# Performance work log

Hardware: AMD Instinct MI355X
Metric: run time of the kernel (lower is better)

The kernel has to match this reference:

```python
import jax, jax.numpy as jnp
import numpy as np

HEADS = 6
WS = 16          # window_size
OWS = 24         # overlap_win_size
DIM = 192
TABLE = (WS + OWS - 1) ** 2  # 1521


def setup_inputs() -> dict:
    key = jax.random.key(0)
    k1, k2, k3, k4, k5, k6 = jax.random.split(key, 6)
    b = 256
    nq = WS * WS          # 256
    n = OWS * OWS         # 576
    x_q = jax.random.normal(k1, (b, nq, DIM), dtype=jnp.float32)
    x_kv = jax.random.normal(k2, (b, n, DIM), dtype=jnp.float32)
    rpi = jax.random.randint(k3, (nq, n), 0, TABLE, dtype=jnp.int64)
    Wq = jax.random.normal(k4, (DIM, DIM), dtype=jnp.float32) * 0.02
    Wkv = jax.random.normal(k5, (2 * DIM, DIM), dtype=jnp.float32) * 0.02
    bias_table = jax.random.normal(k6, (TABLE, HEADS), dtype=jnp.float32) * 0.02
    return {"x_q": x_q, "x_kv": x_kv, "rpi": rpi, "Wq": Wq, "Wkv": Wkv, "bias_table": bias_table}


def reference(x_q, x_kv, rpi, Wq, Wkv, bias_table):
    b, nq, dim = x_q.shape
    n = x_kv.shape[1]
    hd = dim // HEADS
    scale = hd ** (-0.5)

    # projections (torch Linear: y = x @ W^T)
    q = (x_q @ Wq.T).reshape(b, nq, HEADS, hd).transpose(0, 2, 1, 3)      # b h nq d
    kv = x_kv @ Wkv.T                                                    # b n 2*dim
    k, v = jnp.split(kv, 2, axis=-1)
    k = k.reshape(b, n, HEADS, hd).transpose(0, 2, 1, 3)                  # b h n d
    v = v.reshape(b, n, HEADS, hd).transpose(0, 2, 1, 3)                  # b h n d

    attn = scale * jnp.einsum('bhqd,bhkd->bhqk', q, k)                    # b h nq n

    # gathered relative-position bias: table[rpi] -> (nq, n, h)
    rpb = bias_table[rpi.reshape(-1)].reshape(nq, n, HEADS)
    # nq < n branch in source: permute(2, 0, 1) -> (h, nq, n)
    rpb = rpb.transpose(2, 0, 1)

    attn = jax.nn.softmax(attn + rpb[None], axis=-1)
    out = jnp.einsum('bhqk,bhkd->bhqd', attn, v)                          # b h nq d
    out = out.transpose(0, 2, 1, 3).reshape(b, nq, dim)
    return out
```

## Files before the change

### kernel.cpp

```cpp
#include <hip/hip_runtime.h>
#include <cstdint>

typedef unsigned short u16;
typedef short s16x8 __attribute__((ext_vector_type(8)));
typedef float f32x4 __attribute__((ext_vector_type(4)));
typedef float f32x16 __attribute__((ext_vector_type(16)));

#if __has_builtin(__builtin_amdgcn_exp2f)
#define EXP2(x) __builtin_amdgcn_exp2f(x)
#else
#define EXP2(x) __expf((x)*0.6931471805599453f)
#endif

__device__ __forceinline__ u16 f2bf(float x) {
  uint32_t u = __builtin_bit_cast(uint32_t, x);
  u += 0x7FFFu + ((u >> 16) & 1u);
  return (u16)(u >> 16);
}
__device__ __forceinline__ float bf2f(u16 v) {
  return __builtin_bit_cast(float, (uint32_t)v << 16);
}
__device__ __forceinline__ uint32_t pk_bf16(float lo, float hi) {
  uint32_t ul = __builtin_bit_cast(uint32_t, lo);
  uint32_t uh = __builtin_bit_cast(uint32_t, hi);
  ul += 0x7FFFu + ((ul >> 16) & 1u);
  uh += 0x7FFFu + ((uh >> 16) & 1u);
  return __builtin_amdgcn_perm(uh, ul, 0x07060302u);
}
__device__ __forceinline__ f32x4 mfma16(s16x8 a, s16x8 b, f32x4 c) {
  return __builtin_amdgcn_mfma_f32_16x16x32_bf16(a, b, c, 0, 0, 0);
}
__device__ __forceinline__ f32x16 mfma32(s16x8 a, s16x8 b, f32x16 c) {
  return __builtin_amdgcn_mfma_f32_32x32x16_bf16(a, b, c, 0, 0, 0);
}
__device__ __forceinline__ s16x8 ld_frag(const u16* p) {
  uint4 v = *(const uint4*)p;
  return __builtin_bit_cast(s16x8, v);
}

__global__ void prep_w(const float* __restrict__ Wq, const float* __restrict__ Wkv,
                       u16* __restrict__ wqs, u16* __restrict__ wkvs) {
  int tid = blockIdx.x * 256 + threadIdx.x;
  if (tid >= 13824) return;
  bool isQ = tid < 4608;
  int id = isQ ? tid : tid - 4608;
  int lane = id & 63, fk = id >> 6;
  int kk = fk % 6, fb = fk / 6;
  int f = fb * 16 + (lane & 15), k0 = kk * 32 + ((lane >> 4) << 3);
  const float* src = (isQ ? Wq : Wkv) + (size_t)f * 192 + k0;
  const float sc = isQ ? 0.2550348583f : 1.0f;
  float4 a = ((const float4*)src)[0], b = ((const float4*)src)[1];
  uint4 o;
  o.x = pk_bf16(a.x * sc, a.y * sc); o.y = pk_bf16(a.z * sc, a.w * sc);
  o.z = pk_bf16(b.x * sc, b.y * sc); o.w = pk_bf16(b.z * sc, b.w * sc);
  *(uint4*)&(isQ ? wqs : wkvs)[(size_t)id * 8] = o;
}

__global__ void build_rpb(const int* __restrict__ rpi, const float* __restrict__ table,
                          u16* __restrict__ rpb) {
  const int bi = blockIdx.x;
  const int h = bi / 18, kt = bi - h * 18;
  const int t = threadIdx.x, lane = t & 63, w = t >> 6;
  const int u = lane >> 5, l31 = lane & 31;
  const int q = (w << 5) + l31;
  const int n0 = (kt << 5) + (u << 2);
  u16 vals[16];
#pragma unroll
  for (int g = 0; g < 4; ++g) {
    int4 id4 = *(const int4*)&rpi[q * 576 + n0 + (g << 3)];
    vals[(g << 2) + 0] = f2bf(table[id4.x * 6 + h] * 1.4426950409f);
    vals[(g << 2) + 1] = f2bf(table[id4.y * 6 + h] * 1.4426950409f);
    vals[(g << 2) + 2] = f2bf(table[id4.z * 6 + h] * 1.4426950409f);
    vals[(g << 2) + 3] = f2bf(table[id4.w * 6 + h] * 1.4426950409f);
  }
  uint4* dst = (uint4*)&rpb[((size_t)bi * 512 + t) * 16];
  dst[0] = *(uint4*)&vals[0];
  dst[1] = *(uint4*)&vals[8];
}

template <int NC, int MODE>
__device__ __forceinline__ void proj_body(const float* __restrict__ A,
                                          const u16* __restrict__ W,
                                          u16* __restrict__ outQ, u16* __restrict__ outK,
                                          u16* __restrict__ outV, int blk,
                                          u16* __restrict__ lAf) {
  const int t = threadIdx.x, lane = t & 63, w = t >> 6, c = lane & 15, hi = lane >> 4;
  const int mbase0 = blk << 7;
#pragma unroll
  for (int p = 0; p < 2; ++p) {
    const int row = (p << 6) + (t >> 2), cq = t & 3;
    const int fr = row >> 4, cc = row & 15;
    const float* src = A + (size_t)(mbase0 + row) * 192 + (cq << 2);
    const int e0 = (cq & 1) << 2;
#pragma unroll
    for (int i = 0; i < 12; ++i) {
      float4 v = *(const float4*)(src + (i << 4));
      const int kk = i >> 1, h2 = ((i & 1) << 1) + (cq >> 1);
      uint2 pv;
      pv.x = pk_bf16(v.x, v.y);
      pv.y = pk_bf16(v.z, v.w);
      *(uint2*)&lAf[((((fr * 6 + kk) << 6) + (h2 << 4) + cc) << 3) + e0] = pv;
    }
  }
  __syncthreads();
  s16x8 af[2][6];
#pragma unroll
  for (int rg = 0; rg < 2; ++rg)
#pragma unroll
    for (int kk = 0; kk < 6; ++kk)
      af[rg][kk] = ld_frag(&lAf[((((((w << 1) + rg) * 6 + kk) << 6) + lane) << 3)]);

  constexpr int TOT = NC * 6;
  s16x8 wB[3][4];
#pragma unroll
  for (int s0 = 0; s0 < 2; ++s0) {
#pragma unroll
    for (int nb = 0; nb < 4; ++nb)
      wB[s0][nb] = ld_frag(&W[((size_t)((nb * 6 + s0) * 64 + lane)) * 8]);
  }
  f32x4 acc[2][4];
#pragma unroll
  for (int rg = 0; rg < 2; ++rg)
#pragma unroll
    for (int nb = 0; nb < 4; ++nb) acc[rg][nb] = f32x4{0.f, 0.f, 0.f, 0.f};
#pragma unroll
  for (int s = 0; s < TOT; ++s) {
    const int nc = s / 6, kk = s % 6;
    if (s + 2 < TOT) {
      const int s2 = s + 2, nc2 = s2 / 6, kk2 = s2 % 6;
#pragma unroll
      for (int nb = 0; nb < 4; ++nb)
        wB[s2 % 3][nb] = ld_frag(&W[((size_t)((((nc2 << 2) + nb) * 6 + kk2) * 64 + lane)) * 8]);
    }
#pragma unroll
    for (int rg = 0; rg < 2; ++rg)
#pragma unroll
      for (int nb = 0; nb < 4; ++nb)
        acc[rg][nb] = mfma16(wB[s % 3][nb], af[rg][kk], acc[rg][nb]);
    if (kk == 5) {
#pragma unroll
      for (int rg = 0; rg < 2; ++rg) {
        const int m = mbase0 + (w << 5) + (rg << 4) + c;
#pragma unroll
        for (int nb = 0; nb < 4; ++nb) {
          int fb = (nc << 6) + (nb << 4) + (hi << 2);
          uint2 pv;
          pv.x = pk_bf16(acc[rg][nb][0], acc[rg][nb][1]);
          pv.y = pk_bf16(acc[rg][nb][2], acc[rg][nb][3]);
          if (MODE == 0) {
            int b = m >> 8, q = m & 255, hh = fb >> 5, d = fb & 31;
            *(uint2*)&outQ[((((size_t)(b * 6 + hh)) << 8) + q) * 32 + d] = pv;
          } else {
            int b = m / 576, tok = m - b * 576;
            if (fb >= 192) {
              int f2 = fb - 192, hh = f2 >> 5, d = f2 & 31;
              *(uint2*)&outV[(((size_t)(b * 6 + hh)) * 576 + tok) * 32 + d] = pv;
            } else {
              int hh = fb >> 5, dd = fb & 31;
              int half = dd >> 4, uu = (dd >> 3) & 1, e0 = dd & 7;
              int ktt = tok >> 5, lt = tok & 31;
              *(uint2*)&outK[(size_t)((b * 6 + hh) * 18 + ktt) * 1024 +
                             half * 512 + uu * 256 + lt * 8 + e0] = pv;
            }
          }
          acc[rg][nb] = f32x4{0.f, 0.f, 0.f, 0.f};
        }
      }
    }
  }
}

__launch_bounds__(256)
__global__ void proj_all(const float* __restrict__ xq, const float* __restrict__ xkv,
                         const u16* __restrict__ wqs, const u16* __restrict__ wkvs,
                         u16* __restrict__ Qws, u16* __restrict__ Kws,
                         u16* __restrict__ Vws) {
  __shared__ __align__(16) u16 lAf[24576];
  int blk = blockIdx.x;
  if (blk < 512) proj_body<3, 0>(xq, wqs, Qws, nullptr, nullptr, blk, lAf);
  else           proj_body<6, 1>(xkv, wkvs, nullptr, Kws, Vws, blk - 512, lAf);
}

#define VSTR 600
__launch_bounds__(512)
__global__ void attn(const u16* __restrict__ Qws, const u16* __restrict__ Kws,
                     const u16* __restrict__ Vws, const u16* __restrict__ rpb,
                     float* __restrict__ out) {
  __shared__ __align__(16) u16 Vt[32 * VSTR];
  const int bh = blockIdx.x, b = bh / 6, h = bh - b * 6;
  const size_t kvbase = (size_t)bh * 576 * 32;
  const int t = threadIdx.x;
  for (int key = t; key < 576; key += 512) {
    int kk = key & 31, k15 = kk & 15;
    int p = ((kk >> 4) << 4) | (((k15 >> 2) & 1) << 3) | ((k15 >> 3) << 2) | (k15 & 3);
    int col = ((key >> 5) << 5) + p;
    const uint4* src = (const uint4*)&Vws[kvbase + (size_t)key * 32];
    uint4 r[4] = {src[0], src[1], src[2], src[3]};
    const u16* vs = (const u16*)r;
#pragma unroll
    for (int d = 0; d < 32; ++d) Vt[d * VSTR + col] = vs[d];
  }
  const int lane = t & 63, l31 = lane & 31, u = lane >> 5, w = t >> 6;
  const int qg = (w << 5) + l31;
  s16x8 qf[2];
#pragma unroll
  for (int m = 0; m < 2; ++m)
    qf[m] = ld_frag(&Qws[((size_t)bh * 256 + qg) * 32 + (m << 4) + (u << 3)]);
  __syncthreads();
  f32x16 oacc;
#pragma unroll
  for (int r = 0; r < 16; ++r) oacc[r] = 0.f;
  float psum = 0.f;
  const u16* kfb = Kws + (size_t)bh * 18432 + (size_t)lane * 8;
  const u16* bp0 = rpb + (size_t)h * 147456 + (size_t)t * 16;
  s16x8 kA[2], kB[2];
  uint4 bA[2], bB[2];
  kA[0] = ld_frag(kfb);        kB[0] = ld_frag(kfb + 512);
  kA[1] = ld_frag(kfb + 1024); kB[1] = ld_frag(kfb + 1536);
  bA[0] = *(const uint4*)(bp0);        bB[0] = *(const uint4*)(bp0 + 8);
  bA[1] = *(const uint4*)(bp0 + 8192); bB[1] = *(const uint4*)(bp0 + 8192 + 8);
#pragma unroll 2
  for (int kt = 0; kt < 18; ++kt) {
    const int k0 = kt << 5, cur = kt & 1;
    s16x8 vf0 = ld_frag(&Vt[l31 * VSTR + k0 + (u << 3)]);
    s16x8 vf1 = ld_frag(&Vt[l31 * VSTR + k0 + 16 + (u << 3)]);
    f32x16 st;
#pragma unroll
    for (int r = 0; r < 16; ++r) st[r] = 0.f;
    st = mfma32(kA[cur], qf[0], st);
    st = mfma32(kB[cur], qf[1], st);
    uint4 bAc = bA[cur], bBc = bB[cur];
    if (kt < 16) {
      kA[cur] = ld_frag(kfb + (size_t)(kt + 2) * 1024);
      kB[cur] = ld_frag(kfb + (size_t)(kt + 2) * 1024 + 512);
      bA[cur] = *(const uint4*)(bp0 + (size_t)(kt + 2) * 8192);
      bB[cur] = *(const uint4*)(bp0 + (size_t)(kt + 2) * 8192 + 8);
    }
    const u16* b0 = (const u16*)&bAc;
    const u16* b1 = (const u16*)&bBc;
    float e[16];
#pragma unroll
    for (int r = 0; r < 8; ++r)
      e[r] = EXP2(st[r] + bf2f(b0[r]));
#pragma unroll
    for (int r = 8; r < 16; ++r)
      e[r] = EXP2(st[r] + bf2f(b1[r - 8]));
    psum += (((e[0] + e[1]) + (e[2] + e[3])) + ((e[4] + e[5]) + (e[6] + e[7]))) +
            (((e[8] + e[9]) + (e[10] + e[11])) + ((e[12] + e[13]) + (e[14] + e[15])));
    uint4 pa, pb;
    pa.x = pk_bf16(e[0], e[1]);   pa.y = pk_bf16(e[2], e[3]);
    pa.z = pk_bf16(e[4], e[5]);   pa.w = pk_bf16(e[6], e[7]);
    pb.x = pk_bf16(e[8], e[9]);   pb.y = pk_bf16(e[10], e[11]);
    pb.z = pk_bf16(e[12], e[13]); pb.w = pk_bf16(e[14], e[15]);
    s16x8 pf0 = __builtin_bit_cast(s16x8, pa);
    s16x8 pf1 = __builtin_bit_cast(s16x8, pb);
    oacc = mfma32(vf0, pf0, oacc);
    oacc = mfma32(vf1, pf1, oacc);
  }
  float tot = psum + __shfl_xor(psum, 32);
  float rs = 1.0f / tot;
  float* op = out + ((size_t)b * 256 + qg) * 192 + h * 32 + (u << 2);
#pragma unroll
  for (int g = 0; g < 4; ++g) {
    float4 o;
    o.x = oacc[(g << 2) + 0] * rs; o.y = oacc[(g << 2) + 1] * rs;
    o.z = oacc[(g << 2) + 2] * rs; o.w = oacc[(g << 2) + 3] * rs;
    *(float4*)(op + (g << 3)) = o;
  }
}

extern "C" void kernel_launch(void* const* d_in, const int* in_sizes, int n_in,
                              void* d_out, int out_size, void* d_ws, size_t ws_size,
                              hipStream_t stream) {
  const float* x_q   = (const float*)d_in[0];
  const float* x_kv  = (const float*)d_in[1];
  const int*   rpi   = (const int*)d_in[2];
  const float* Wq    = (const float*)d_in[3];
  const float* Wkv   = (const float*)d_in[4];
  const float* table = (const float*)d_in[5];
  float* out = (float*)d_out;

  char* ws = (char*)d_ws;
  u16* wqs  = (u16*)(ws);
  u16* wkvs = (u16*)(ws + 73728);
  u16* rpb  = (u16*)(ws + 221184);
  u16* Qws  = (u16*)(ws + 1990656);
  u16* Kws  = (u16*)(ws + 27156480);
  u16* Vws  = (u16*)(ws + 83779584);

  prep_w<<<54, 256, 0, stream>>>(Wq, Wkv, wqs, wkvs);
  build_rpb<<<108, 512, 0, stream>>>(rpi, table, rpb);
  proj_all<<<1664, 256, 0, stream>>>(x_q, x_kv, wqs, wkvs, Qws, Kws, Vws);
  attn<<<1536, 512, 0, stream>>>(Qws, Kws, Vws, rpb, out);
}
```

Measured before the change: 360.6 us.

## Shrink projection tile to 16 rows per wave with wave-private LDS staging

Each wave in the projection kernel now stages and computes only its own 16-row A tile in a private LDS slice, so the block-wide __syncthreads is replaced by a per-wave lgkmcnt wait. Blocks cover 64 rows instead of 128, which doubles the grid and halves LDS per block. The aim is more parallelism and occupancy and less barrier stalling. The cost is that each weight fragment loaded from global/L2 is reused across half as many rows, roughly doubling weight-load traffic.

```diff
diff --git a/kernel.cpp b/kernel.cpp
--- a/kernel.cpp
+++ b/kernel.cpp
@@ -85,12 +85,11 @@
                                           u16* __restrict__ outV, int blk,
                                           u16* __restrict__ lAf) {
   const int t = threadIdx.x, lane = t & 63, w = t >> 6, c = lane & 15, hi = lane >> 4;
-  const int mbase0 = blk << 7;
-#pragma unroll
-  for (int p = 0; p < 2; ++p) {
-    const int row = (p << 6) + (t >> 2), cq = t & 3;
-    const int fr = row >> 4, cc = row & 15;
-    const float* src = A + (size_t)(mbase0 + row) * 192 + (cq << 2);
+  const int mbase = (blk << 6) + (w << 4);
+  u16* wlds = lAf + w * 3072;
+  {
+    const int r = lane >> 2, cq = lane & 3;
+    const float* src = A + (size_t)(mbase + r) * 192 + (cq << 2);
     const int e0 = (cq & 1) << 2;
 #pragma unroll
     for (int i = 0; i < 12; ++i) {
@@ -99,18 +98,18 @@
       uint2 pv;
       pv.x = pk_bf16(v.x, v.y);
       pv.y = pk_bf16(v.z, v.w);
-      *(uint2*)&lAf[((((fr * 6 + kk) << 6) + (h2 << 4) + cc) << 3) + e0] = pv;
-    }
-  }
-  __syncthreads();
-  s16x8 af[2][6];
-#pragma unroll
-  for (int rg = 0; rg < 2; ++rg)
-#pragma unroll
-    for (int kk = 0; kk < 6; ++kk)
-      af[rg][kk] = ld_frag(&lAf[((((((w << 1) + rg) * 6 + kk) << 6) + lane) << 3)]);
+      *(uint2*)&wlds[(((kk << 6) + (h2 << 4) + r) << 3) + e0] = pv;
+    }
+  }
+  asm volatile("s_waitcnt lgkmcnt(0)" ::: "memory");
+  __builtin_amdgcn_sched_barrier(0);
+  s16x8 af[6];
+#pragma unroll
+  for (int kk = 0; kk < 6; ++kk)
+    af[kk] = ld_frag(&wlds[((kk << 6) + lane) << 3]);
 
   constexpr int TOT = NC * 6;
+  const int m = mbase + c;
   s16x8 wB[3][4];
 #pragma unroll
   for (int s0 = 0; s0 < 2; ++s0) {
@@ -118,11 +117,9 @@
     for (int nb = 0; nb < 4; ++nb)
       wB[s0][nb] = ld_frag(&W[((size_t)((nb * 6 + s0) * 64 + lane)) * 8]);
   }
-  f32x4 acc[2][4];
-#pragma unroll
-  for (int rg = 0; rg < 2; ++rg)
-#pragma unroll
-    for (int nb = 0; nb < 4; ++nb) acc[rg][nb] = f32x4{0.f, 0.f, 0.f, 0.f};
+  f32x4 acc[4];
+#pragma unroll
+  for (int nb = 0; nb < 4; ++nb) acc[nb] = f32x4{0.f, 0.f, 0.f, 0.f};
 #pragma unroll
   for (int s = 0; s < TOT; ++s) {
     const int nc = s / 6, kk = s % 6;
@@ -133,38 +130,32 @@
         wB[s2 % 3][nb] = ld_frag(&W[((size_t)((((nc2 << 2) + nb) * 6 + kk2) * 64 + lane)) * 8]);
     }
 #pragma unroll
-    for (int rg = 0; rg < 2; ++rg)
-#pragma unroll
-      for (int nb = 0; nb < 4; ++nb)
-        acc[rg][nb] = mfma16(wB[s % 3][nb], af[rg][kk], acc[rg][nb]);
+    for (int nb = 0; nb < 4; ++nb)
+      acc[nb] = mfma16(wB[s % 3][nb], af[kk], acc[nb]);
     if (kk == 5) {
 #pragma unroll
-      for (int rg = 0; rg < 2; ++rg) {
-        const int m = mbase0 + (w << 5) + (rg << 4) + c;
-#pragma unroll
-        for (int nb = 0; nb < 4; ++nb) {
-          int fb = (nc << 6) + (nb << 4) + (hi << 2);
-          uint2 pv;
-          pv.x = pk_bf16(acc[rg][nb][0], acc[rg][nb][1]);
-          pv.y = pk_bf16(acc[rg][nb][2], acc[rg][nb][3]);
-          if (MODE == 0) {
-            int b = m >> 8, q = m & 255, hh = fb >> 5, d = fb & 31;
-            *(uint2*)&outQ[((((size_t)(b * 6 + hh)) << 8) + q) * 32 + d] = pv;
+      for (int nb = 0; nb < 4; ++nb) {
+        int fb = (nc << 6) + (nb << 4) + (hi << 2);
+        uint2 pv;
+        pv.x = pk_bf16(acc[nb][0], acc[nb][1]);
+        pv.y = pk_bf16(acc[nb][2], acc[nb][3]);
+        if (MODE == 0) {
+          int b = m >> 8, q = m & 255, hh = fb >> 5, d = fb & 31;
+          *(uint2*)&outQ[((((size_t)(b * 6 + hh)) << 8) + q) * 32 + d] = pv;
+        } else {
+          int b = m / 576, tok = m - b * 576;
+          if (fb >= 192) {
+            int f2 = fb - 192, hh = f2 >> 5, d = f2 & 31;
+            *(uint2*)&outV[(((size_t)(b * 6 + hh)) * 576 + tok) * 32 + d] = pv;
           } else {
-            int b = m / 576, tok = m - b * 576;
-            if (fb >= 192) {
-              int f2 = fb - 192, hh = f2 >> 5, d = f2 & 31;
-              *(uint2*)&outV[(((size_t)(b * 6 + hh)) * 576 + tok) * 32 + d] = pv;
-            } else {
-              int hh = fb >> 5, dd = fb & 31;
-              int half = dd >> 4, uu = (dd >> 3) & 1, e0 = dd & 7;
-              int ktt = tok >> 5, lt = tok & 31;
-              *(uint2*)&outK[(size_t)((b * 6 + hh) * 18 + ktt) * 1024 +
-                             half * 512 + uu * 256 + lt * 8 + e0] = pv;
-            }
+            int hh = fb >> 5, dd = fb & 31;
+            int half = dd >> 4, uu = (dd >> 3) & 1, e0 = dd & 7;
+            int ktt = tok >> 5, lt = tok & 31;
+            *(uint2*)&outK[(size_t)((b * 6 + hh) * 18 + ktt) * 1024 +
+                           half * 512 + uu * 256 + lt * 8 + e0] = pv;
           }
-          acc[rg][nb] = f32x4{0.f, 0.f, 0.f, 0.f};
         }
+        acc[nb] = f32x4{0.f, 0.f, 0.f, 0.f};
       }
     }
   }
@@ -175,10 +166,10 @@
                          const u16* __restrict__ wqs, const u16* __restrict__ wkvs,
                          u16* __restrict__ Qws, u16* __restrict__ Kws,
                          u16* __restrict__ Vws) {
-  __shared__ __align__(16) u16 lAf[24576];
+  __shared__ __align__(16) u16 lAf[12288];
   int blk = blockIdx.x;
-  if (blk < 512) proj_body<3, 0>(xq, wqs, Qws, nullptr, nullptr, blk, lAf);
-  else           proj_body<6, 1>(xkv, wkvs, nullptr, Kws, Vws, blk - 512, lAf);
+  if (blk < 1024) proj_body<3, 0>(xq, wqs, Qws, nullptr, nullptr, blk, lAf);
+  else            proj_body<6, 1>(xkv, wkvs, nullptr, Kws, Vws, blk - 1024, lAf);
 }
 
 #define VSTR 600
@@ -290,6 +281,6 @@
 
   prep_w<<<54, 256, 0, stream>>>(Wq, Wkv, wqs, wkvs);
   build_rpb<<<108, 512, 0, stream>>>(rpi, table, rpb);
-  proj_all<<<1664, 256, 0, stream>>>(x_q, x_kv, wqs, wkvs, Qws, Kws, Vws);
+  proj_all<<<3328, 256, 0, stream>>>(x_q, x_kv, wqs, wkvs, Qws, Kws, Vws);
   attn<<<1536, 512, 0, stream>>>(Qws, Kws, Vws, rpb, out);
 }
```

New measurement: 361.2 us. Within noise of the previous version (+0.2%).
